# Performance work log

Hardware: AMD Instinct MI355X
Metric: run time of the kernel (lower is better)

## Reference

```python
import jax, jax.numpy as jnp
import numpy as np


def setup_inputs() -> dict:
    key = jax.random.key(0)
    ks = jax.random.split(key, 5)
    B, N, D = 32, 128, 4096
    return {
        "curr_head": jax.random.normal(ks[0], (B, D), jnp.float32),
        "curr_errors": jax.random.normal(ks[1], (B, N, D), jnp.float32),
        "curr_head_2": jax.random.normal(ks[2], (B, D), jnp.float32),
        "curr_errors_2": jax.random.normal(ks[3], (B, N, D), jnp.float32),
        "adv_errors": jax.random.normal(ks[4], (B, N, D), jnp.float32),
        "shared_errors": 128,
    }


def reference(curr_head, curr_errors, curr_head_2, curr_errors_2, adv_errors, shared_errors):
    B = curr_head.shape[0]
    tail = curr_head.shape[1:]
    # (B, N, *tail) -> (N, B, *tail), matching torch's view + transpose(1, 0)
    e1 = jnp.moveaxis(curr_errors.reshape(B, -1, *tail), 1, 0)
    e2 = jnp.moveaxis(curr_errors_2.reshape(B, -1, *tail), 1, 0)
    N1, N2 = e1.shape[0], e2.shape[0]
    s = int(shared_errors)

    def zeros(n):
        return jnp.zeros((n, B) + tail, e1.dtype)

    # self_errors / factor_errors: (N1 + N2 - s, B, *tail)
    self_errors = jnp.concatenate([e1, zeros(N2 - s)], axis=0)
    factor_errors = jnp.concatenate([e2[:s], zeros(N1 - s), e2[s:]], axis=0)

    lin_err = curr_head[None] * factor_errors + curr_head_2[None] * self_errors
    quadr_const = self_errors * factor_errors

    # Exact identity: 0.5*sum_ij |a_i a_j + a_j a_i| = (sum_i |a_i|)^2 (elementwise),
    # since a_i*a_j is already symmetric. Avoids the (N,N,B,*tail) outer product.
    abs_sum = jnp.abs(self_errors).sum(axis=0)
    quadr_error = abs_sum * abs_sum - 0.5 * jnp.abs(quadr_const).sum(axis=0)

    new_head = curr_head * curr_head_2 + 0.5 * quadr_const.sum(axis=0)

    errors = jnp.moveaxis(lin_err, 0, 1)  # (B, N1+N2-s, *tail)
    new_errors = jnp.concatenate([errors, quadr_error[:, None] * adv_errors], axis=1)
    new_errors = new_errors.reshape(-1, *tail)
    return new_head, new_errors
```

## Files before the change

kernel.cpp:

```cpp
#include <hip/hip_runtime.h>

constexpr int B  = 32;
constexpr int N  = 128;
constexpr int D  = 4096;
constexpr int DV = D / 4;
constexpr int COLS   = 64;
constexpr int CHUNKS = 16;
constexpr int NPC    = N / CHUNKS;
constexpr int TPB    = COLS * CHUNKS;
constexpr int TILES  = DV / COLS;

typedef float f4 __attribute__((ext_vector_type(4)));

__device__ __forceinline__ f4 f4abs(f4 a) {
    f4 r;
    r.x = fabsf(a.x); r.y = fabsf(a.y); r.z = fabsf(a.z); r.w = fabsf(a.w);
    return r;
}

__global__ __launch_bounds__(TPB) void relaxed_prod_kernel(
    const float* __restrict__ h1,
    const float* __restrict__ e1,
    const float* __restrict__ h2,
    const float* __restrict__ e2,
    const float* __restrict__ adv,
    float* __restrict__ out)
{
    const int lane  = threadIdx.x & (COLS - 1);
    const int chunk = threadIdx.x / COLS;
    const int tile  = blockIdx.x % TILES;
    const int b     = blockIdx.x / TILES;
    const long d0   = ((long)tile * COLS + lane) * 4;

    const f4* e1p  = (const f4*)(e1  + (long)b * N * D + d0);
    const f4* e2p  = (const f4*)(e2  + (long)b * N * D + d0);
    const f4* advp = (const f4*)(adv + (long)b * N * D + d0);
    f4* lin_out = (f4*)(out + (long)B * D + (long)b * (2 * N) * D + d0);
    f4* adv_out = lin_out + (long)N * DV;

    const f4 vh1 = *(const f4*)(h1 + (long)b * D + d0);
    const f4 vh2 = *(const f4*)(h2 + (long)b * D + d0);

    f4 sq  = (f4)(0.f);
    f4 sa  = (f4)(0.f);
    f4 saq = (f4)(0.f);

    const int n0 = chunk * NPC;
#pragma unroll
    for (int i = 0; i < NPC; i += 2) {
        const long off0 = (long)(n0 + i) * DV;
        const long off1 = (long)(n0 + i + 1) * DV;
        f4 a0 = e1p[off0];
        f4 f0 = e2p[off0];
        f4 a1 = e1p[off1];
        f4 f1 = e2p[off1];

        f4 lin0 = vh1 * f0 + vh2 * a0;
        f4 lin1 = vh1 * f1 + vh2 * a1;
        __builtin_nontemporal_store(lin0, &lin_out[off0]);
        __builtin_nontemporal_store(lin1, &lin_out[off1]);

        f4 q0 = a0 * f0;
        f4 q1 = a1 * f1;
        sq  += q0 + q1;
        sa  += f4abs(a0) + f4abs(a1);
        saq += f4abs(q0) + f4abs(q1);
    }

    __shared__ f4 s_q [CHUNKS][COLS];
    __shared__ f4 s_a [CHUNKS][COLS];
    __shared__ f4 s_aq[CHUNKS][COLS];
    __shared__ f4 s_qe[COLS];
    s_q [chunk][lane] = sq;
    s_a [chunk][lane] = sa;
    s_aq[chunk][lane] = saq;
    __syncthreads();

    if (chunk == 0) {
        f4 tq  = s_q [0][lane];
        f4 ta  = s_a [0][lane];
        f4 taq = s_aq[0][lane];
#pragma unroll
        for (int c = 1; c < CHUNKS; ++c) {
            tq  += s_q [c][lane];
            ta  += s_a [c][lane];
            taq += s_aq[c][lane];
        }
        f4 qe = ta * ta - 0.5f * taq;
        f4 nh = vh1 * vh2 + 0.5f * tq;
        *(f4*)(out + (long)b * D + d0) = nh;
        s_qe[lane] = qe;
    }
    __syncthreads();

    const f4 qe = s_qe[lane];
#pragma unroll
    for (int i = 0; i < NPC; i += 2) {
        const long off0 = (long)(n0 + i) * DV;
        const long off1 = (long)(n0 + i + 1) * DV;
        f4 v0 = advp[off0];
        f4 v1 = advp[off1];
        __builtin_nontemporal_store(qe * v0, &adv_out[off0]);
        __builtin_nontemporal_store(qe * v1, &adv_out[off1]);
    }
}

extern "C" void kernel_launch(void* const* d_in, const int* in_sizes, int n_in,
                              void* d_out, int out_size, void* d_ws, size_t ws_size,
                              hipStream_t stream) {
    const float* h1  = (const float*)d_in[0];
    const float* e1  = (const float*)d_in[1];
    const float* h2  = (const float*)d_in[2];
    const float* e2  = (const float*)d_in[3];
    const float* adv = (const float*)d_in[4];
    float* out = (float*)d_out;

    dim3 grid(B * TILES);
    dim3 block(TPB);
    relaxed_prod_kernel<<<grid, block, 0, stream>>>(h1, e1, h2, e2, adv, out);
}
```

Measured before the change: 286.4 us.

## Split fused kernel into lin, reduce, finalize and adv kernels via workspace

Replaces the single fused kernel with four launches: an elementwise lin kernel, a partial reduction over N into a workspace, a finalize kernel for new_head and quadr_error, and an elementwise adv-scaling kernel. The aim is simpler, fully parallel elementwise kernels without block-level syncs between phases. In exchange, e1 and e2 are read twice (once for lin, once for the reduction), there are extra launches and a workspace round trip, and nontemporal stores are dropped. The original fused kernel is kept as a fallback for when the workspace is too small.

Result: slower. 304.7 us (+6.4%).

```diff
diff --git a/kernel.cpp b/kernel.cpp
--- a/kernel.cpp
+++ b/kernel.cpp
@@ -4,11 +4,8 @@
 constexpr int N  = 128;
 constexpr int D  = 4096;
 constexpr int DV = D / 4;
-constexpr int COLS   = 64;
-constexpr int CHUNKS = 16;
-constexpr int NPC    = N / CHUNKS;
-constexpr int TPB    = COLS * CHUNKS;
-constexpr int TILES  = DV / COLS;
+constexpr int TOT = B * N * DV;
+constexpr long ASZ = (long)B * 4 * DV;
 
 typedef float f4 __attribute__((ext_vector_type(4)));
 
@@ -18,104 +15,158 @@
     return r;
 }
 
-__global__ __launch_bounds__(TPB) void relaxed_prod_kernel(
-    const float* __restrict__ h1,
-    const float* __restrict__ e1,
-    const float* __restrict__ h2,
-    const float* __restrict__ e2,
-    const float* __restrict__ adv,
-    float* __restrict__ out)
+__global__ __launch_bounds__(256) void k_lin(
+    const f4* __restrict__ h1, const f4* __restrict__ e1,
+    const f4* __restrict__ h2, const f4* __restrict__ e2,
+    f4* __restrict__ out)
 {
-    const int lane  = threadIdx.x & (COLS - 1);
-    const int chunk = threadIdx.x / COLS;
-    const int tile  = blockIdx.x % TILES;
-    const int b     = blockIdx.x / TILES;
-    const long d0   = ((long)tile * COLS + lane) * 4;
+    const int id = blockIdx.x * 256 + threadIdx.x;
+    const int c  = id & (DV - 1);
+    const int bn = id >> 10;
+    const int b  = bn >> 7;
+    const int hc = (b << 10) + c;
+    f4 a = e1[id];
+    f4 f = e2[id];
+    out[(long)B * DV + ((long)(bn + (b << 7)) << 10) + c] = h1[hc] * f + h2[hc] * a;
+}
+
+__global__ __launch_bounds__(256) void k_red(
+    const f4* __restrict__ e1, const f4* __restrict__ e2, f4* __restrict__ ws)
+{
+    const int blk = blockIdx.x;
+    const int b   = blk >> 4;
+    const int r   = blk & 15;
+    const int dt  = r & 3;
+    const int nq  = r >> 2;
+    const int c0  = dt * 256 + threadIdx.x;
+    const long base = ((long)(b * N + nq * 32) << 10) + c0;
+    const f4* p1 = e1 + base;
+    const f4* p2 = e2 + base;
+
+    f4 sq  = {0.f, 0.f, 0.f, 0.f};
+    f4 sa  = {0.f, 0.f, 0.f, 0.f};
+    f4 saq = {0.f, 0.f, 0.f, 0.f};
+#pragma unroll 8
+    for (int i = 0; i < 32; ++i) {
+        f4 a = p1[(long)i << 10];
+        f4 f = p2[(long)i << 10];
+        f4 q = a * f;
+        sq  += q;
+        sa  += f4abs(a);
+        saq += f4abs(q);
+    }
+    const long pb = ((long)(b * 4 + nq) << 10) + c0;
+    ws[pb]            = sq;
+    ws[ASZ + pb]      = sa;
+    ws[2 * ASZ + pb]  = saq;
+}
+
+__global__ __launch_bounds__(256) void k_fin(
+    const f4* __restrict__ h1, const f4* __restrict__ h2,
+    f4* __restrict__ out, f4* __restrict__ ws)
+{
+    const int id = blockIdx.x * 256 + threadIdx.x;
+    const int b  = id >> 10;
+    const int c  = id & (DV - 1);
+    f4 tq  = {0.f, 0.f, 0.f, 0.f};
+    f4 ta  = {0.f, 0.f, 0.f, 0.f};
+    f4 taq = {0.f, 0.f, 0.f, 0.f};
+#pragma unroll
+    for (int q = 0; q < 4; ++q) {
+        const long p = ((long)(b * 4 + q) << 10) + c;
+        tq  += ws[p];
+        ta  += ws[ASZ + p];
+        taq += ws[2 * ASZ + p];
+    }
+    out[id] = h1[id] * h2[id] + 0.5f * tq;
+    ws[3 * ASZ + id] = ta * ta - 0.5f * taq;
+}
+
+__global__ __launch_bounds__(256) void k_adv(
+    const f4* __restrict__ adv, f4* __restrict__ out, const f4* __restrict__ ws)
+{
+    const int id = blockIdx.x * 256 + threadIdx.x;
+    const int c  = id & (DV - 1);
+    const int bn = id >> 10;
+    const int b  = bn >> 7;
+    f4 qe = ws[3 * ASZ + (b << 10) + c];
+    out[(long)B * DV + ((long)(bn + (b << 7) + N) << 10) + c] = qe * adv[id];
+}
+
+constexpr int FB_COLS = 64, FB_CHUNKS = 16, FB_NPC = N / FB_CHUNKS,
+              FB_TPB = FB_COLS * FB_CHUNKS, FB_TILES = DV / FB_COLS;
+
+__global__ __launch_bounds__(FB_TPB) void relaxed_prod_fallback(
+    const float* __restrict__ h1, const float* __restrict__ e1,
+    const float* __restrict__ h2, const float* __restrict__ e2,
+    const float* __restrict__ adv, float* __restrict__ out)
+{
+    const int lane  = threadIdx.x & (FB_COLS - 1);
+    const int chunk = threadIdx.x / FB_COLS;
+    const int tile  = blockIdx.x % FB_TILES;
+    const int b     = blockIdx.x / FB_TILES;
+    const long d0   = ((long)tile * FB_COLS + lane) * 4;
 
     const f4* e1p  = (const f4*)(e1  + (long)b * N * D + d0);
     const f4* e2p  = (const f4*)(e2  + (long)b * N * D + d0);
     const f4* advp = (const f4*)(adv + (long)b * N * D + d0);
     f4* lin_out = (f4*)(out + (long)B * D + (long)b * (2 * N) * D + d0);
     f4* adv_out = lin_out + (long)N * DV;
-
     const f4 vh1 = *(const f4*)(h1 + (long)b * D + d0);
     const f4 vh2 = *(const f4*)(h2 + (long)b * D + d0);
 
-    f4 sq  = (f4)(0.f);
-    f4 sa  = (f4)(0.f);
-    f4 saq = (f4)(0.f);
-
-    const int n0 = chunk * NPC;
+    f4 sq = {0,0,0,0}, sa = {0,0,0,0}, saq = {0,0,0,0};
+    const int n0 = chunk * FB_NPC;
 #pragma unroll
-    for (int i = 0; i < NPC; i += 2) {
-        const long off0 = (long)(n0 + i) * DV;
-        const long off1 = (long)(n0 + i + 1) * DV;
-        f4 a0 = e1p[off0];
-        f4 f0 = e2p[off0];
-        f4 a1 = e1p[off1];
-        f4 f1 = e2p[off1];
-
-        f4 lin0 = vh1 * f0 + vh2 * a0;
-        f4 lin1 = vh1 * f1 + vh2 * a1;
-        __builtin_nontemporal_store(lin0, &lin_out[off0]);
-        __builtin_nontemporal_store(lin1, &lin_out[off1]);
-
-        f4 q0 = a0 * f0;
-        f4 q1 = a1 * f1;
-        sq  += q0 + q1;
-        sa  += f4abs(a0) + f4abs(a1);
-        saq += f4abs(q0) + f4abs(q1);
+    for (int i = 0; i < FB_NPC; ++i) {
+        const long off = (long)(n0 + i) * DV;
+        f4 a = e1p[off], f = e2p[off];
+        lin_out[off] = vh1 * f + vh2 * a;
+        f4 q = a * f;
+        sq += q; sa += f4abs(a); saq += f4abs(q);
     }
-
-    __shared__ f4 s_q [CHUNKS][COLS];
-    __shared__ f4 s_a [CHUNKS][COLS];
-    __shared__ f4 s_aq[CHUNKS][COLS];
-    __shared__ f4 s_qe[COLS];
-    s_q [chunk][lane] = sq;
-    s_a [chunk][lane] = sa;
-    s_aq[chunk][lane] = saq;
+    __shared__ f4 s_q[FB_CHUNKS][FB_COLS], s_a[FB_CHUNKS][FB_COLS],
+                  s_aq[FB_CHUNKS][FB_COLS], s_qe[FB_COLS];
+    s_q[chunk][lane] = sq; s_a[chunk][lane] = sa; s_aq[chunk][lane] = saq;
     __syncthreads();
-
     if (chunk == 0) {
-        f4 tq  = s_q [0][lane];
-        f4 ta  = s_a [0][lane];
-        f4 taq = s_aq[0][lane];
+        f4 tq = s_q[0][lane], ta = s_a[0][lane], taq = s_aq[0][lane];
 #pragma unroll
-        for (int c = 1; c < CHUNKS; ++c) {
-            tq  += s_q [c][lane];
-            ta  += s_a [c][lane];
-            taq += s_aq[c][lane];
+        for (int cc = 1; cc < FB_CHUNKS; ++cc) {
+            tq += s_q[cc][lane]; ta += s_a[cc][lane]; taq += s_aq[cc][lane];
         }
-        f4 qe = ta * ta - 0.5f * taq;
-        f4 nh = vh1 * vh2 + 0.5f * tq;
-        *(f4*)(out + (long)b * D + d0) = nh;
-        s_qe[lane] = qe;
+        *(f4*)(out + (long)b * D + d0) = vh1 * vh2 + 0.5f * tq;
+        s_qe[lane] = ta * ta - 0.5f * taq;
     }
     __syncthreads();
-
     const f4 qe = s_qe[lane];
 #pragma unroll
-    for (int i = 0; i < NPC; i += 2) {
-        const long off0 = (long)(n0 + i) * DV;
-        const long off1 = (long)(n0 + i + 1) * DV;
-        f4 v0 = advp[off0];
-        f4 v1 = advp[off1];
-        __builtin_nontemporal_store(qe * v0, &adv_out[off0]);
-        __builtin_nontemporal_store(qe * v1, &adv_out[off1]);
+    for (int i = 0; i < FB_NPC; ++i) {
+        const long off = (long)(n0 + i) * DV;
+        adv_out[off] = qe * advp[off];
     }
 }
 
 extern "C" void kernel_launch(void* const* d_in, const int* in_sizes, int n_in,
                               void* d_out, int out_size, void* d_ws, size_t ws_size,
                               hipStream_t stream) {
-    const float* h1  = (const float*)d_in[0];
-    const float* e1  = (const float*)d_in[1];
-    const float* h2  = (const float*)d_in[2];
-    const float* e2  = (const float*)d_in[3];
-    const float* adv = (const float*)d_in[4];
-    float* out = (float*)d_out;
+    const f4* h1  = (const f4*)d_in[0];
+    const f4* e1  = (const f4*)d_in[1];
+    const f4* h2  = (const f4*)d_in[2];
+    const f4* e2  = (const f4*)d_in[3];
+    const f4* adv = (const f4*)d_in[4];
+    f4* out = (f4*)d_out;
+    f4* ws  = (f4*)d_ws;
 
-    dim3 grid(B * TILES);
-    dim3 block(TPB);
-    relaxed_prod_kernel<<<grid, block, 0, stream>>>(h1, e1, h2, e2, adv, out);
+    const size_t ws_need = (size_t)(3 * ASZ + (long)B * DV) * sizeof(f4);
+    if (ws_size >= ws_need) {
+        k_lin<<<dim3(TOT / 256), dim3(256), 0, stream>>>(h1, e1, h2, e2, out);
+        k_red<<<dim3(512), dim3(256), 0, stream>>>(e1, e2, ws);
+        k_fin<<<dim3(B * DV / 256), dim3(256), 0, stream>>>(h1, h2, out, ws);
+        k_adv<<<dim3(TOT / 256), dim3(256), 0, stream>>>(adv, out, ws);
+    } else {
+        relaxed_prod_fallback<<<dim3(B * FB_TILES), dim3(FB_TPB), 0, stream>>>(
+            (const float*)d_in[0], (const float*)d_in[1], (const float*)d_in[2],
+            (const float*)d_in[3], (const float*)d_in[4], (float*)d_out);
+    }
 }
```

## Halve chunks per block and double-buffer row loads in registers

Applied to the files above, without the earlier changes.

Each block now runs 8 chunks instead of 16, so every thread handles 16 rows instead of 8. Row loads are grouped into batches of 4 and register double-buffered, so the next batch's global loads are issued before the current batch is computed and stored. Both the error loop and the adv loop get this prefetch. The nontemporal store builtin is replaced with plain stores, which may change cache behaviour for the large output. Register pressure also rises and there are fewer threads per block.

Measured after the change: 285.4 us. Within noise of the previous version (-0.3%).

```diff
diff --git a/kernel.cpp b/kernel.cpp
--- a/kernel.cpp
+++ b/kernel.cpp
@@ -5,8 +5,10 @@
 constexpr int D  = 4096;
 constexpr int DV = D / 4;
 constexpr int COLS   = 64;
-constexpr int CHUNKS = 16;
+constexpr int CHUNKS = 8;
 constexpr int NPC    = N / CHUNKS;
+constexpr int BATCH  = 4;
+constexpr int NBT    = NPC / BATCH;
 constexpr int TPB    = COLS * CHUNKS;
 constexpr int TILES  = DV / COLS;
 
@@ -46,25 +48,36 @@
     f4 saq = (f4)(0.f);
 
     const int n0 = chunk * NPC;
+
+    f4 Aa[2][BATCH], Ff[2][BATCH];
 #pragma unroll
-    for (int i = 0; i < NPC; i += 2) {
-        const long off0 = (long)(n0 + i) * DV;
-        const long off1 = (long)(n0 + i + 1) * DV;
-        f4 a0 = e1p[off0];
-        f4 f0 = e2p[off0];
-        f4 a1 = e1p[off1];
-        f4 f1 = e2p[off1];
-
-        f4 lin0 = vh1 * f0 + vh2 * a0;
-        f4 lin1 = vh1 * f1 + vh2 * a1;
-        __builtin_nontemporal_store(lin0, &lin_out[off0]);
-        __builtin_nontemporal_store(lin1, &lin_out[off1]);
-
-        f4 q0 = a0 * f0;
-        f4 q1 = a1 * f1;
-        sq  += q0 + q1;
-        sa  += f4abs(a0) + f4abs(a1);
-        saq += f4abs(q0) + f4abs(q1);
+    for (int j = 0; j < BATCH; ++j) {
+        const long off = (long)(n0 + j) * DV;
+        Aa[0][j] = e1p[off];
+        Ff[0][j] = e2p[off];
+    }
+#pragma unroll
+    for (int bt = 0; bt < NBT; ++bt) {
+        const int cur = bt & 1, nxt = cur ^ 1;
+        if (bt < NBT - 1) {
+#pragma unroll
+            for (int j = 0; j < BATCH; ++j) {
+                const long off = (long)(n0 + (bt + 1) * BATCH + j) * DV;
+                Aa[nxt][j] = e1p[off];
+                Ff[nxt][j] = e2p[off];
+            }
+        }
+#pragma unroll
+        for (int j = 0; j < BATCH; ++j) {
+            const long off = (long)(n0 + bt * BATCH + j) * DV;
+            f4 a = Aa[cur][j];
+            f4 f = Ff[cur][j];
+            lin_out[off] = vh1 * f + vh2 * a;
+            f4 q = a * f;
+            sq  += q;
+            sa  += f4abs(a);
+            saq += f4abs(q);
+        }
     }
 
     __shared__ f4 s_q [CHUNKS][COLS];
@@ -94,14 +107,23 @@
     __syncthreads();
 
     const f4 qe = s_qe[lane];
+    f4 Vv[2][BATCH];
 #pragma unroll
-    for (int i = 0; i < NPC; i += 2) {
-        const long off0 = (long)(n0 + i) * DV;
-        const long off1 = (long)(n0 + i + 1) * DV;
-        f4 v0 = advp[off0];
-        f4 v1 = advp[off1];
-        __builtin_nontemporal_store(qe * v0, &adv_out[off0]);
-        __builtin_nontemporal_store(qe * v1, &adv_out[off1]);
+    for (int j = 0; j < BATCH; ++j)
+        Vv[0][j] = advp[(long)(n0 + j) * DV];
+#pragma unroll
+    for (int bt = 0; bt < NBT; ++bt) {
+        const int cur = bt & 1, nxt = cur ^ 1;
+        if (bt < NBT - 1) {
+#pragma unroll
+            for (int j = 0; j < BATCH; ++j)
+                Vv[nxt][j] = advp[(long)(n0 + (bt + 1) * BATCH + j) * DV];
+        }
+#pragma unroll
+        for (int j = 0; j < BATCH; ++j) {
+            const long off = (long)(n0 + bt * BATCH + j) * DV;
+            adv_out[off] = qe * Vv[cur][j];
+        }
     }
 }
 
```
